# Kernel tuning notes

Measured on AMD Instinct MI355X. Metric: run time of the kernel, lower is better.

Reference implementation:

```python
import jax, jax.numpy as jnp
import numpy as np

L = 5          # number of pyramid levels (cat_fuse expects 5*C input channels)
C = 192        # in_channels, divisible by 3 and 2
C3 = C // 3
C2 = C // 2
B = 4
SIZES = [(192, 192), (96, 96), (48, 48), (24, 24), (12, 12)]  # x[1] is reference scale


def conv1x1(x, w, b):
    # 1x1 conv (+ folded eval-mode BN): x [n,cin,h,w], w [cout,cin], b [cout]
    return jnp.einsum('oc,nchw->nohw', w, x) + b[None, :, None, None]


def setup_inputs() -> dict:
    key = jax.random.key(0)
    ks = iter(jax.random.split(key, 40))
    inp = {}
    for i, (h, w) in enumerate(SIZES):
        inp[f'x{i}'] = jax.random.normal(next(ks), (B, C, h, w), jnp.float32)
    def wp(shape):
        return jax.random.normal(next(ks), shape, jnp.float32) * 0.05
    for nm, co, ci in [('k1', C3, C), ('k2', C3, C), ('k3', C3, C), ('q', C, C), ('v', C, C),
                       ('cf', C, L * C), ('e1', C2, C), ('e2', C, C2), ('r1', C2, C), ('r2', C, C2)]:
        inp['W_' + nm] = wp((co, ci))
        inp['b_' + nm] = wp((co,))
    inp['bn_s'] = 1.0 + wp((C,))   # standalone BN folded to affine scale
    inp['bn_t'] = wp((C,))         # standalone BN folded to affine shift
    return inp


def reference(x0, x1, x2, x3, x4,
              W_k1, b_k1, W_k2, b_k2, W_k3, b_k3,
              W_q, b_q, W_v, b_v, W_cf, b_cf,
              W_e1, b_e1, W_e2, b_e2, W_r1, b_r1, W_r2, b_r2,
              bn_s, bn_t):
    xs = [x0, x1, x2, x3, x4]
    b, _, h, w = x1.shape
    hw = h * w
    # bilinear resize to reference scale (torch F.interpolate align_corners=False)
    x_up = [x1 if i == 1 else jax.image.resize(x, (b, C, h, w), 'bilinear') for i, x in enumerate(xs)]
    Xf = jnp.stack(x_up).reshape(L * b, C, h, w)  # shared weights across levels -> batch them

    def emb(z):  # conv1x1 -> GELU(exact) -> conv1x1 (dropout is identity at eval)
        return conv1x1(jax.nn.gelu(conv1x1(z, W_e1, b_e1), approximate=False), W_e2, b_e2)

    la_res = None
    for k in range(5):
        # residual refinement: relu(bn(x + res_block(x)))
        r = conv1x1(jax.nn.relu(conv1x1(Xf, W_r1, b_r1)), W_r2, b_r2)
        Xf = jax.nn.relu((Xf + r) * bn_s[None, :, None, None] + bn_t[None, :, None, None])
        # query/value: per-level projection, split C into 3 chunks -> 15 'keys' per pixel
        Q = conv1x1(Xf, W_q, b_q).reshape(L, b, 3, C3, hw)
        Q = Q.transpose(1, 0, 2, 3, 4).reshape(b, 3 * L, C3, hw).transpose(0, 3, 2, 1)  # [b,hw,C3,15]
        V = conv1x1(Xf, W_v, b_v).reshape(L, b, 3, C3, hw)
        V = V.transpose(1, 0, 2, 3, 4).reshape(b, 3 * L, C3, hw).transpose(0, 3, 1, 2)  # [b,hw,15,C3]
        if k == 0:
            cat = Xf.reshape(L, b, C, h, w).transpose(1, 0, 2, 3, 4).reshape(b, L * C, h, w)
            la_res = emb(jax.nn.relu(conv1x1(cat, W_cf, b_cf)))
        refs = []
        for Wk, bk in ((W_k1, b_k1), (W_k2, b_k2), (W_k3, b_k3)):
            key_i = conv1x1(la_res, Wk, bk).reshape(b, C3, hw).transpose(0, 2, 1)       # [b,hw,C3]
            att = jax.nn.softmax(jnp.einsum('bpc,bpck->bpk', key_i, Q), axis=-1)        # [b,hw,15]
            ref = jnp.einsum('bpk,bpkc->bpc', att, V)                                   # [b,hw,C3]
            refs.append(ref.transpose(0, 2, 1).reshape(b, C3, h, w))
        la_res = emb(jnp.concatenate(refs, axis=1))
    return la_res
```

## Files before the change

kernel.cpp:

```cpp
#include <hip/hip_runtime.h>
#include <math.h>

typedef unsigned short u16;
typedef unsigned int   u32;
typedef __bf16 bf16x8 __attribute__((ext_vector_type(8)));
typedef float  f32x4  __attribute__((ext_vector_type(4)));

__device__ __forceinline__ float b2f(u16 u) {
    unsigned v = ((unsigned)u) << 16;
    return __uint_as_float(v);
}
__device__ __forceinline__ u16 f2b(float f) {
    unsigned x = __float_as_uint(f);
    unsigned r = (x + 0x7fffu + ((x >> 16) & 1u)) >> 16;
    return (u16)r;
}
__device__ __forceinline__ void fsplit(float v, u16& h, u16& l) {
    h = f2b(v);
    l = f2b(v - b2f(h));
}
__device__ __forceinline__ float h2f(u16 u) {
    union { u16 us; _Float16 h; } c; c.us = u; return (float)c.h;
}
__device__ __forceinline__ u16 f2h(float f) {
    union { u16 us; _Float16 h; } c; c.h = (_Float16)f; return c.us;
}
__device__ __forceinline__ float ldx(const void* p, size_t i, int f32m) {
    return f32m ? ((const float*)p)[i] : b2f(((const u16*)p)[i]);
}

__global__ void detect_dtype(const u16* __restrict__ x0, int* flag)
{
    int lane = threadIdx.x;
    int bad = 0;
    for (int i = lane; i < 1024; i += 64) {
        float v = b2f(x0[i]);
        if (!(fabsf(v) < 32768.f)) bad = 1;
    }
    unsigned long long m = __ballot(bad);
    if (lane == 0) flag[0] = (m != 0ULL) ? 1 : 0;
}

struct SrcPtrs {
    const void *wr1, *br1, *wr2, *br2, *wq, *bq, *wv, *bv, *wcf, *bcf;
    const void *we1, *be1, *we2, *be2, *wk1, *bk1, *wk2, *bk2, *wk3, *bk3;
    const void *bns, *bnt;
};
__global__ void pack_weights(SrcPtrs S, u16* __restrict__ Wh, u16* __restrict__ Wl,
                             float* __restrict__ Bias, const int* __restrict__ dflag)
{
    const int f32m = *dflag;
    int idx = blockIdx.x * 256 + threadIdx.x;
    if (idx < 368640) {
        const void* src; size_t si;
        if (idx < 18432)       { src = S.wr1; si = idx; }
        else if (idx < 36864)  { src = S.wr2; si = idx - 18432; }
        else if (idx < 110592) {
            int r = idx - 36864, o = r / 192, c = r % 192;
            if (o < 192) { src = S.wq; si = (size_t)o * 192 + c; }
            else         { src = S.wv; si = (size_t)(o - 192) * 192 + c; }
        }
        else if (idx < 294912) { src = S.wcf; si = idx - 110592; }
        else if (idx < 313344) { src = S.we1; si = idx - 294912; }
        else if (idx < 331776) { src = S.we2; si = idx - 313344; }
        else {
            int r = idx - 331776, o = r / 192, c = r % 192;
            src = (o < 64) ? S.wk1 : ((o < 128) ? S.wk2 : S.wk3);
            si = (size_t)(o & 63) * 192 + c;
        }
        u16 h, l; fsplit(ldx(src, si, f32m), h, l);
        Wh[idx] = h; Wl[idx] = l;
    } else if (idx < 370368) {
        int b = idx - 368640; const void* src; size_t si;
        if (b < 96)        { src = S.br1; si = b; }
        else if (b < 288)  { src = S.br2; si = b - 96; }
        else if (b < 672)  { int r = b - 288;
                             if (r < 192) { src = S.bq; si = r; }
                             else         { src = S.bv; si = r - 192; } }
        else if (b < 864)  { src = S.bcf; si = b - 672; }
        else if (b < 960)  { src = S.be1; si = b - 864; }
        else if (b < 1152) { src = S.be2; si = b - 960; }
        else if (b < 1344) { int r = b - 1152;
                             src = (r < 64) ? S.bk1 : ((r < 128) ? S.bk2 : S.bk3);
                             si = r & 63; }
        else if (b < 1536) { src = S.bns; si = b - 1344; }
        else               { src = S.bnt; si = b - 1536; }
        Bias[b] = ldx(src, si, f32m);
    }
}

__global__ void build_tables(float* __restrict__ wtab, int* __restrict__ jtab)
{
    int t = threadIdx.x;
    if (t >= 384) return;
    int li = t / 96, o = t % 96;
    const int ins[4] = {192, 48, 24, 12};
    int in = ins[li];
    float scale = (float)in / 96.0f;
    float ksc = fmaxf(scale, 1.0f);
    float cc = (o + 0.5f) * scale - 0.5f;
    float w[4] = {0.f, 0.f, 0.f, 0.f};
    int   j[4] = {0, 0, 0, 0};
    int n = 0; float s = 0.f;
    int jl = (int)floorf(cc - ksc), jh = (int)floorf(cc + ksc) + 1;
    for (int jj = jl; jj <= jh; jj++) {
        if (jj < 0 || jj >= in) continue;
        float ww = 1.0f - fabsf((float)jj - cc) / ksc;
        if (ww <= 0.f) continue;
        if (n < 4) { w[n] = ww; j[n] = jj; s += ww; n++; }
    }
    for (int i = 0; i < 4; i++) {
        wtab[li * 384 + o * 4 + i] = w[i] / s;
        jtab[li * 384 + o * 4 + i] = j[i];
    }
}

template<int SPLIT>
__launch_bounds__(256)
__global__ void transpose_in(const void* __restrict__ src, int HW,
                             u32* __restrict__ P, u16* __restrict__ Xh,
                             u16* __restrict__ Xl, const int* __restrict__ dflag)
{
    __shared__ float t[32][33];
    const int f32m = *dflag;
    const int b  = blockIdx.z;
    const int c0 = blockIdx.y * 32;
    const int p0 = blockIdx.x * 32;
    const int tid = threadIdx.x;
#pragma unroll
    for (int it = 0; it < 4; it++) {
        int i = it * 256 + tid;
        int pl = i & 31, cl = i >> 5;
        int p = p0 + pl;
        float v = 0.f;
        if (p < HW) v = ldx(src, ((size_t)(b * 192 + c0 + cl)) * HW + p, f32m);
        t[pl][cl] = v;
    }
    __syncthreads();
#pragma unroll
    for (int it = 0; it < 4; it++) {
        int i = it * 256 + tid;
        int cl = i & 31, pl = i >> 5;
        int p = p0 + pl;
        if (p >= HW) continue;
        float v = t[pl][cl];
        u16 h, l; fsplit(v, h, l);
        if constexpr (SPLIT) {
            size_t oi = ((size_t)((4 + b) * 9216 + p)) * 192 + c0 + cl;
            Xh[oi] = h; Xl[oi] = l;
        } else {
            P[((size_t)b * HW + p) * 192 + c0 + cl] = (u32)h | ((u32)l << 16);
        }
    }
}

template<int TAPS>
__launch_bounds__(256)
__global__ void upsample2(const u32* __restrict__ Pa, const u32* __restrict__ Pb,
                          const u32* __restrict__ Pc,
                          const float* __restrict__ wtab, const int* __restrict__ jtab,
                          u16* __restrict__ Xh, u16* __restrict__ Xl)
{
    int li, b, l, in;
    const u32* P;
    if constexpr (TAPS == 4) {
        li = 0; b = blockIdx.y; l = 0; in = 192; P = Pa;
    } else {
        int yi = blockIdx.y;
        li = 1 + (yi >> 2); b = yi & 3;
        const int lvl[4] = {0, 2, 3, 4};
        const int ins[4] = {192, 48, 24, 12};
        l = lvl[li]; in = ins[li];
        P = (li == 1) ? Pa : ((li == 2) ? Pb : Pc);
    }
    int gid = blockIdx.x * 256 + threadIdx.x;
    int c = gid % 192;
    int p = gid / 192;
    int y = p / 96, x = p % 96;
    const float* wt = wtab + li * 384;
    const int*   jt = jtab + li * 384;

    size_t ib = (size_t)b * in * in * 192 + c;
    float a = 0.f;
#pragma unroll
    for (int iy = 0; iy < TAPS; iy++) {
        float wy = wt[y * 4 + iy];
        size_t rb = ib + (size_t)(jt[y * 4 + iy] * in) * 192;
        float ax = 0.f;
#pragma unroll
        for (int ix = 0; ix < TAPS; ix++) {
            u32 u = P[rb + jt[x * 4 + ix] * 192];
            ax += wt[x * 4 + ix] * (b2f((u16)u) + b2f((u16)(u >> 16)));
        }
        a += wy * ax;
    }
    size_t oi = ((size_t)(l * 4 + b) * 9216 + p) * 192 + c;
    u16 h, lo; fsplit(a, h, lo);
    Xh[oi] = h; Xl[oi] = lo;
}

template<int MT, int NT, int ACT, int MODE, int OUT>
__launch_bounds__(256)
__global__ void conv_gemm(const u16* __restrict__ Ah, const u16* __restrict__ Al,
                          const u16* __restrict__ Wh, const u16* __restrict__ Wl,
                          const float* __restrict__ Bias,
                          int woff, int boff, int K, int O,
                          u16* __restrict__ out0, u16* __restrict__ out1)
{
    constexpr int BM = MT * 64, BN = NT * 16;
    __shared__ u16 Ash[BM * 40];
    __shared__ u16 Asl[BM * 40];
    __shared__ u16 Bsh[BN * 40];
    __shared__ u16 Bsl[BN * 40];

    const int tid  = threadIdx.x;
    const int lane = tid & 63, wave = tid >> 6;
    const int qd   = lane >> 4, ln = lane & 15;
    const int p0   = blockIdx.x * BM;
    const int img  = blockIdx.z;
    const int M    = 9216;

    f32x4 acc[MT][NT];
#pragma unroll
    for (int mt = 0; mt < MT; mt++)
#pragma unroll
        for (int j = 0; j < NT; j++) acc[mt][j] = (f32x4){0.f, 0.f, 0.f, 0.f};

    for (int kb = 0; kb < K; kb += 32) {
#pragma unroll
        for (int i = 0; i < MT; i++) {
            int idx = i * 256 + tid;
            int row = idx >> 2, ch = idx & 3;
            size_t base;
            if constexpr (MODE == 2) {
                int l = kb / 192, c0 = kb - l * 192 + ch * 8;
                base = ((size_t)((l * 4 + img) * M + p0 + row)) * 192 + c0;
            } else {
                base = ((size_t)(img * M + p0 + row)) * (size_t)K + kb + ch * 8;
            }
            *(float4*)&Ash[row * 40 + ch * 8] = *(const float4*)(Ah + base);
            *(float4*)&Asl[row * 40 + ch * 8] = *(const float4*)(Al + base);
        }
        constexpr int BI = (BN * 4) / 256;
#pragma unroll
        for (int i = 0; i < BI; i++) {
            int idx = i * 256 + tid;
            int row = idx >> 2, ch = idx & 3;
            size_t wb = (size_t)woff + (size_t)row * K + kb + ch * 8;
            *(float4*)&Bsh[row * 40 + ch * 8] = *(const float4*)(Wh + wb);
            *(float4*)&Bsl[row * 40 + ch * 8] = *(const float4*)(Wl + wb);
        }
        __syncthreads();
        bf16x8 ah[MT], al[MT];
#pragma unroll
        for (int mt = 0; mt < MT; mt++) {
            ah[mt] = *(const bf16x8*)&Ash[(wave * MT * 16 + mt * 16 + ln) * 40 + qd * 8];
            al[mt] = *(const bf16x8*)&Asl[(wave * MT * 16 + mt * 16 + ln) * 40 + qd * 8];
        }
#pragma unroll
        for (int j = 0; j < NT; j++) {
            bf16x8 bh = *(const bf16x8*)&Bsh[(j * 16 + ln) * 40 + qd * 8];
            bf16x8 bl = *(const bf16x8*)&Bsl[(j * 16 + ln) * 40 + qd * 8];
#pragma unroll
            for (int mt = 0; mt < MT; mt++) {
                acc[mt][j] = __builtin_amdgcn_mfma_f32_16x16x32_bf16(ah[mt], bh, acc[mt][j], 0, 0, 0);
                acc[mt][j] = __builtin_amdgcn_mfma_f32_16x16x32_bf16(ah[mt], bl, acc[mt][j], 0, 0, 0);
                acc[mt][j] = __builtin_amdgcn_mfma_f32_16x16x32_bf16(al[mt], bh, acc[mt][j], 0, 0, 0);
            }
        }
        __syncthreads();
    }

#pragma unroll
    for (int mt = 0; mt < MT; mt++) {
#pragma unroll
        for (int j = 0; j < NT; j++) {
            int o = j * 16 + ln;
            float bvf = Bias[boff + o];
#pragma unroll
            for (int r = 0; r < 4; r++) {
                int prow = p0 + wave * MT * 16 + mt * 16 + qd * 4 + r;
                float v = acc[mt][j][r] + bvf;
                if constexpr (ACT == 1) v = fmaxf(v, 0.f);
                if constexpr (OUT == 0) {
                    size_t oidx = ((size_t)(img * M + prow)) * (size_t)O + o;
                    u16 h, l; fsplit(v, h, l);
                    out0[oidx] = h; out1[oidx] = l;
                } else if constexpr (OUT == 1) {
                    out0[((size_t)(img * M + prow)) * (size_t)O + o] = f2h(v);
                } else {
                    size_t pb = ((size_t)(img * M + prow)) * 192;
                    if (o < 192) out0[pb + o] = f2h(v);
                    else         out1[pb + o - 192] = f2h(v);
                }
            }
        }
    }
}

template<int ACT1, int MODE2>
__launch_bounds__(256)
__global__ void fused_mlp(const u16* __restrict__ Ah, const u16* __restrict__ Al,
                          const u16* __restrict__ Wh, const u16* __restrict__ Wl,
                          const float* __restrict__ Bias,
                          int w1off, int b1off, int w2off, int b2off,
                          u16* __restrict__ outh, u16* __restrict__ outl)
{
    __shared__ u16 Hh[64 * 104];
    __shared__ u16 Hl[64 * 104];
    __shared__ u16 SB[15360];
    u16* B1h = SB;
    u16* B1l = SB + 3840;
    u16* As  = SB + 7680;
    u16* Asl = SB + 10240;

    const int tid  = threadIdx.x;
    const int lane = tid & 63, wave = tid >> 6;
    const int qd   = lane >> 4, ln = lane & 15;
    const int p0   = blockIdx.x * 64;
    const int img  = blockIdx.z;
    const int M    = 9216;

    f32x4 acc1[6];
#pragma unroll
    for (int j = 0; j < 6; j++) acc1[j] = (f32x4){0.f, 0.f, 0.f, 0.f};

    for (int kb = 0; kb < 192; kb += 32) {
        {
            int row = tid >> 2, ch = tid & 3;
            size_t base = ((size_t)(img * M + p0 + row)) * 192 + kb + ch * 8;
            *(float4*)&As[row * 40 + ch * 8]  = *(const float4*)(Ah + base);
            *(float4*)&Asl[row * 40 + ch * 8] = *(const float4*)(Al + base);
        }
#pragma unroll
        for (int i = 0; i < 2; i++) {
            int idx = i * 256 + tid;
            if (idx < 384) {
                int row = idx >> 2, ch = idx & 3;
                size_t wb = (size_t)w1off + (size_t)row * 192 + kb + ch * 8;
                *(float4*)&B1h[row * 40 + ch * 8] = *(const float4*)(Wh + wb);
                *(float4*)&B1l[row * 40 + ch * 8] = *(const float4*)(Wl + wb);
            }
        }
        __syncthreads();
        bf16x8 ah = *(const bf16x8*)&As[(wave * 16 + ln) * 40 + qd * 8];
        bf16x8 al = *(const bf16x8*)&Asl[(wave * 16 + ln) * 40 + qd * 8];
#pragma unroll
        for (int j = 0; j < 6; j++) {
            bf16x8 bh = *(const bf16x8*)&B1h[(j * 16 + ln) * 40 + qd * 8];
            bf16x8 bl = *(const bf16x8*)&B1l[(j * 16 + ln) * 40 + qd * 8];
            acc1[j] = __builtin_amdgcn_mfma_f32_16x16x32_bf16(ah, bh, acc1[j], 0, 0, 0);
            acc1[j] = __builtin_amdgcn_mfma_f32_16x16x32_bf16(ah, bl, acc1[j], 0, 0, 0);
            acc1[j] = __builtin_amdgcn_mfma_f32_16x16x32_bf16(al, bh, acc1[j], 0, 0, 0);
        }
        __syncthreads();
    }
#pragma unroll
    for (int j = 0; j < 6; j++) {
        int o = j * 16 + ln;
        float bvf = Bias[b1off + o];
#pragma unroll
        for (int r = 0; r < 4; r++) {
            float v = acc1[j][r] + bvf;
            if constexpr (ACT1 == 1) v = fmaxf(v, 0.f);
            if constexpr (ACT1 == 2) v = 0.5f * v * (1.f + erff(v * 0.70710678118654752f));
            u16 h, l; fsplit(v, h, l);
            int row = wave * 16 + qd * 4 + r;
            Hh[row * 104 + o] = h;
            Hl[row * 104 + o] = l;
        }
    }
    __syncthreads();

    u16* B2h = SB;
    u16* B2l = SB + 7680;
    f32x4 acc2[12];
#pragma unroll
    for (int j = 0; j < 12; j++) acc2[j] = (f32x4){0.f, 0.f, 0.f, 0.f};

    for (int kb = 0; kb < 96; kb += 32) {
#pragma unroll
        for (int i = 0; i < 3; i++) {
            int idx = i * 256 + tid;
            int row = idx >> 2, ch = idx & 3;
            size_t wb = (size_t)w2off + (size_t)row * 96 + kb + ch * 8;
            *(float4*)&B2h[row * 40 + ch * 8] = *(const float4*)(Wh + wb);
            *(float4*)&B2l[row * 40 + ch * 8] = *(const float4*)(Wl + wb);
        }
        __syncthreads();
        bf16x8 ah = *(const bf16x8*)&Hh[(wave * 16 + ln) * 104 + kb + qd * 8];
        bf16x8 al = *(const bf16x8*)&Hl[(wave * 16 + ln) * 104 + kb + qd * 8];
#pragma unroll
        for (int j = 0; j < 12; j++) {
            bf16x8 bh = *(const bf16x8*)&B2h[(j * 16 + ln) * 40 + qd * 8];
            bf16x8 bl = *(const bf16x8*)&B2l[(j * 16 + ln) * 40 + qd * 8];
            acc2[j] = __builtin_amdgcn_mfma_f32_16x16x32_bf16(ah, bh, acc2[j], 0, 0, 0);
            acc2[j] = __builtin_amdgcn_mfma_f32_16x16x32_bf16(ah, bl, acc2[j], 0, 0, 0);
            acc2[j] = __builtin_amdgcn_mfma_f32_16x16x32_bf16(al, bh, acc2[j], 0, 0, 0);
        }
        __syncthreads();
    }

#pragma unroll
    for (int j = 0; j < 12; j++) {
        int o = j * 16 + ln;
        float bvf = Bias[b2off + o];
#pragma unroll
        for (int r = 0; r < 4; r++) {
            int prow = p0 + wave * 16 + qd * 4 + r;
            float v = acc2[j][r] + bvf;
            size_t oidx = ((size_t)(img * M + prow)) * 192 + o;
            if constexpr (MODE2 == 1) {
                float xo = b2f(outh[oidx]) + b2f(outl[oidx]);
                v = fmaxf((xo + v) * Bias[1344 + o] + Bias[1536 + o], 0.f);
            }
            u16 h, l; fsplit(v, h, l);
            outh[oidx] = h; outl[oidx] = l;
        }
    }
}

template<int WRITE_X>
__launch_bounds__(256)
__global__ void fused_res_qv(u16* __restrict__ Xh, u16* __restrict__ Xl,
                             const u16* __restrict__ Wh, const u16* __restrict__ Wl,
                             const float* __restrict__ Bias,
                             u16* __restrict__ Qf, u16* __restrict__ Vf)
{
    __shared__ __align__(16) u16 LDS[39936];
    u16* Hh  = LDS;
    u16* Hl  = LDS + 6656;
    u16* SB  = LDS + 13312;
    u16* B1h = SB;
    u16* B1l = SB + 3840;
    u16* As  = SB + 7680;
    u16* Asl = SB + 10240;

    const int tid  = threadIdx.x;
    const int lane = tid & 63, wave = tid >> 6;
    const int qd   = lane >> 4, ln = lane & 15;
    const int p0   = blockIdx.x * 64;
    const int img  = blockIdx.z;
    const int M    = 9216;

    f32x4 acc1[6];
#pragma unroll
    for (int j = 0; j < 6; j++) acc1[j] = (f32x4){0.f, 0.f, 0.f, 0.f};

    for (int kb = 0; kb < 192; kb += 32) {
        {
            int row = tid >> 2, ch = tid & 3;
            size_t base = ((size_t)(img * M + p0 + row)) * 192 + kb + ch * 8;
            *(float4*)&As[row * 40 + ch * 8]  = *(const float4*)(Xh + base);
            *(float4*)&Asl[row * 40 + ch * 8] = *(const float4*)(Xl + base);
        }
#pragma unroll
        for (int i = 0; i < 2; i++) {
            int idx = i * 256 + tid;
            if (idx < 384) {
                int row = idx >> 2, ch = idx & 3;
                size_t wb = (size_t)row * 192 + kb + ch * 8;
                *(float4*)&B1h[row * 40 + ch * 8] = *(const float4*)(Wh + wb);
                *(float4*)&B1l[row * 40 + ch * 8] = *(const float4*)(Wl + wb);
            }
        }
        __syncthreads();
        bf16x8 ah = *(const bf16x8*)&As[(wave * 16 + ln) * 40 + qd * 8];
        bf16x8 al = *(const bf16x8*)&Asl[(wave * 16 + ln) * 40 + qd * 8];
#pragma unroll
        for (int j = 0; j < 6; j++) {
            bf16x8 bh = *(const bf16x8*)&B1h[(j * 16 + ln) * 40 + qd * 8];
            bf16x8 bl = *(const bf16x8*)&B1l[(j * 16 + ln) * 40 + qd * 8];
            acc1[j] = __builtin_amdgcn_mfma_f32_16x16x32_bf16(ah, bh, acc1[j], 0, 0, 0);
            acc1[j] = __builtin_amdgcn_mfma_f32_16x16x32_bf16(ah, bl, acc1[j], 0, 0, 0);
            acc1[j] = __builtin_amdgcn_mfma_f32_16x16x32_bf16(al, bh, acc1[j], 0, 0, 0);
        }
        __syncthreads();
    }
#pragma unroll
    for (int j = 0; j < 6; j++) {
        int o = j * 16 + ln;
        float bvf = Bias[o];
#pragma unroll
        for (int r = 0; r < 4; r++) {
            float v = fmaxf(acc1[j][r] + bvf, 0.f);
            u16 h, l; fsplit(v, h, l);
            int row = wave * 16 + qd * 4 + r;
            Hh[row * 104 + o] = h;
            Hl[row * 104 + o] = l;
        }
    }
    __syncthreads();

    u16* B2h = SB;
    u16* B2l = SB + 7680;
    f32x4 acc2[12];
#pragma unroll
    for (int j = 0; j < 12; j++) acc2[j] = (f32x4){0.f, 0.f, 0.f, 0.f};

    for (int kb = 0; kb < 96; kb += 32) {
#pragma unroll
        for (int i = 0; i < 3; i++) {
            int idx = i * 256 + tid;
            int row = idx >> 2, ch = idx & 3;
            size_t wb = (size_t)18432 + (size_t)row * 96 + kb + ch * 8;
            *(float4*)&B2h[row * 40 + ch * 8] = *(const float4*)(Wh + wb);
            *(float4*)&B2l[row * 40 + ch * 8] = *(const float4*)(Wl + wb);
        }
        __syncthreads();
        bf16x8 ah = *(const bf16x8*)&Hh[(wave * 16 + ln) * 104 + kb + qd * 8];
        bf16x8 al = *(const bf16x8*)&Hl[(wave * 16 + ln) * 104 + kb + qd * 8];
#pragma unroll
        for (int j = 0; j < 12; j++) {
            bf16x8 bh = *(const bf16x8*)&B2h[(j * 16 + ln) * 40 + qd * 8];
            bf16x8 bl = *(const bf16x8*)&B2l[(j * 16 + ln) * 40 + qd * 8];
            acc2[j] = __builtin_amdgcn_mfma_f32_16x16x32_bf16(ah, bh, acc2[j], 0, 0, 0);
            acc2[j] = __builtin_amdgcn_mfma_f32_16x16x32_bf16(ah, bl, acc2[j], 0, 0, 0);
            acc2[j] = __builtin_amdgcn_mfma_f32_16x16x32_bf16(al, bh, acc2[j], 0, 0, 0);
        }
        __syncthreads();
    }

    u16* X2h = LDS;
    u16* X2l = LDS + 12288;
#pragma unroll
    for (int j = 0; j < 12; j++) {
        int o = j * 16 + ln;
        float bvf = Bias[96 + o];
#pragma unroll
        for (int r = 0; r < 4; r++) {
            int row  = wave * 16 + qd * 4 + r;
            int prow = p0 + row;
            float v = acc2[j][r] + bvf;
            size_t oidx = ((size_t)(img * M + prow)) * 192 + o;
            float xo = b2f(Xh[oidx]) + b2f(Xl[oidx]);
            v = fmaxf((xo + v) * Bias[1344 + o] + Bias[1536 + o], 0.f);
            u16 h, l; fsplit(v, h, l);
            if constexpr (WRITE_X) { Xh[oidx] = h; Xl[oidx] = l; }
            int off = ((row * 192 + o) * 2) ^ ((row & 7) << 4);
            *(u16*)((char*)X2h + off) = h;
            *(u16*)((char*)X2l + off) = l;
        }
    }
    __syncthreads();

    u16* B3h = LDS + 24576;
    u16* B3l = LDS + 32256;
    const int arow = wave * 16 + ln;
#pragma unroll 1
    for (int pass = 0; pass < 2; pass++) {
        f32x4 acc3[12];
#pragma unroll
        for (int j = 0; j < 12; j++) acc3[j] = (f32x4){0.f, 0.f, 0.f, 0.f};

        for (int kb = 0; kb < 192; kb += 32) {
#pragma unroll
            for (int i = 0; i < 3; i++) {
                int idx = i * 256 + tid;
                int row = idx >> 2, ch = idx & 3;
                size_t wb = (size_t)36864 + (size_t)(pass * 192 + row) * 192 + kb + ch * 8;
                *(float4*)&B3h[row * 40 + ch * 8] = *(const float4*)(Wh + wb);
                *(float4*)&B3l[row * 40 + ch * 8] = *(const float4*)(Wl + wb);
            }
            __syncthreads();
            int aoff = ((arow * 192 + kb + qd * 8) * 2) ^ ((arow & 7) << 4);
            bf16x8 ah = *(const bf16x8*)((const char*)X2h + aoff);
            bf16x8 al = *(const bf16x8*)((const char*)X2l + aoff);
#pragma unroll
            for (int j = 0; j < 12; j++) {
                bf16x8 bh = *(const bf16x8*)&B3h[(j * 16 + ln) * 40 + qd * 8];
                bf16x8 bl = *(const bf16x8*)&B3l[(j * 16 + ln) * 40 + qd * 8];
                acc3[j] = __builtin_amdgcn_mfma_f32_16x16x32_bf16(ah, bh, acc3[j], 0, 0, 0);
                acc3[j] = __builtin_amdgcn_mfma_f32_16x16x32_bf16(ah, bl, acc3[j], 0, 0, 0);
                acc3[j] = __builtin_amdgcn_mfma_f32_16x16x32_bf16(al, bh, acc3[j], 0, 0, 0);
            }
            __syncthreads();
        }
#pragma unroll
        for (int j = 0; j < 12; j++) {
            int o = pass * 192 + j * 16 + ln;
            float bvf = Bias[288 + o];
#pragma unroll
            for (int r = 0; r < 4; r++) {
                int prow = p0 + wave * 16 + qd * 4 + r;
                float v = acc3[j][r] + bvf;
                u16 q = f2h(v);
                size_t pb = ((size_t)(img * M + prow)) * 192;
                if (o < 192) Qf[pb + o] = q;
                else         Vf[pb + o - 192] = q;
            }
        }
    }
}

__global__ void attn_kernel(const u16* __restrict__ Qb, const u16* __restrict__ Vb,
                            const u16* __restrict__ Keys,
                            u16* __restrict__ Rh, u16* __restrict__ Rl)
{
    const int lane = threadIdx.x & 63;
    const int wv   = threadIdx.x >> 6;
    const int p = blockIdx.x * 4 + wv;
    const int b = blockIdx.y;

    float qv[15], vv[15];
#pragma unroll
    for (int l = 0; l < 5; l++) {
        size_t base = ((size_t)((l * 4 + b) * 9216 + p)) * 192;
#pragma unroll
        for (int j = 0; j < 3; j++) {
            qv[l * 3 + j] = h2f(Qb[base + j * 64 + lane]);
            vv[l * 3 + j] = h2f(Vb[base + j * 64 + lane]);
        }
    }
    size_t kb = ((size_t)(b * 9216 + p)) * 192;
#pragma unroll
    for (int i = 0; i < 3; i++) {
        float kf = h2f(Keys[kb + i * 64 + lane]);
        float lg[15];
#pragma unroll
        for (int t = 0; t < 15; t++) {
            float s = kf * qv[t];
#pragma unroll
            for (int m = 1; m < 64; m <<= 1) s += __shfl_xor(s, m, 64);
            lg[t] = s;
        }
        float mx = lg[0];
#pragma unroll
        for (int t = 1; t < 15; t++) mx = fmaxf(mx, lg[t]);
        float sum = 0.f;
#pragma unroll
        for (int t = 0; t < 15; t++) { lg[t] = __expf(lg[t] - mx); sum += lg[t]; }
        float inv = 1.f / sum;
        float ref = 0.f;
#pragma unroll
        for (int t = 0; t < 15; t++) ref += lg[t] * vv[t];
        u16 h, lo; fsplit(ref * inv, h, lo);
        Rh[kb + i * 64 + lane] = h;
        Rl[kb + i * 64 + lane] = lo;
    }
}

__launch_bounds__(256)
__global__ void transpose_out(const u16* __restrict__ Lah, const u16* __restrict__ Lal,
                              float* __restrict__ out)
{
    __shared__ float t[32][33];
    const int b  = blockIdx.z;
    const int c0 = blockIdx.y * 32;
    const int p0 = blockIdx.x * 32;
    const int tid = threadIdx.x;
#pragma unroll
    for (int it = 0; it < 4; it++) {
        int i = it * 256 + tid;
        int cl = i & 31, pl = i >> 5;
        size_t idx = ((size_t)(b * 9216 + p0 + pl)) * 192 + c0 + cl;
        t[pl][cl] = b2f(Lah[idx]) + b2f(Lal[idx]);
    }
    __syncthreads();
#pragma unroll
    for (int it = 0; it < 4; it++) {
        int i = it * 256 + tid;
        int pl = i & 31, cl = i >> 5;
        out[((size_t)(b * 192 + c0 + cl)) * 9216 + p0 + pl] = t[pl][cl];
    }
}

__global__ void ws_too_small_kernel(float* out)
{
    int gid = blockIdx.x * 256 + threadIdx.x;
    out[gid] = 12345.0f;
}

extern "C" void kernel_launch(void* const* d_in, const int* in_sizes, int n_in,
                              void* d_out, int out_size, void* d_ws, size_t ws_size,
                              hipStream_t stream)
{
    u16* ws = (u16*)d_ws;
    const size_t oXh   = 0;
    const size_t oXl   = 35389440;
    const size_t oQ    = 70778880;
    const size_t oV    = 106168320;
    const size_t oLah  = 141557760;
    const size_t oLal  = 148635648;
    const size_t oKeys = 155713536;
    const size_t oRh   = 162791424;
    const size_t oRl   = 169869312;
    const size_t oWh   = 176947200;
    const size_t oWl   = 177315840;
    const size_t oBias = 177684480;
    const size_t oWtab = 177687936;
    const size_t oJtab = 177691008;
    const size_t oFlag = 177694080;
    const size_t need_bytes = (size_t)177694096 * 2;

    if (ws_size < need_bytes) {
        ws_too_small_kernel<<<dim3(out_size / 256), dim3(256), 0, stream>>>((float*)d_out);
        return;
    }

    u16* Xh   = ws + oXh;
    u16* Xl   = ws + oXl;
    u16* Qf   = ws + oQ;
    u16* Vf   = ws + oV;
    u16* Lah  = ws + oLah;
    u16* Lal  = ws + oLal;
    u16* Keys = ws + oKeys;
    u16* Rh   = ws + oRh;
    u16* Rl   = ws + oRl;
    u16* Wh   = ws + oWh;
    u16* Wl   = ws + oWl;
    float* Bias = (float*)(ws + oBias);
    float* wtab = (float*)(ws + oWtab);
    int*   jtab = (int*)(ws + oJtab);
    int*   flag = (int*)(ws + oFlag);

    u32* P0 = (u32*)(ws + oQ);
    u32* P2 = (u32*)(ws + oLah);
    u32* P3 = (u32*)(ws + oLal);
    u32* P4 = (u32*)(ws + oKeys);

    SrcPtrs S;
    S.wk1 = d_in[5];  S.bk1 = d_in[6];
    S.wk2 = d_in[7];  S.bk2 = d_in[8];
    S.wk3 = d_in[9];  S.bk3 = d_in[10];
    S.wq  = d_in[11]; S.bq  = d_in[12];
    S.wv  = d_in[13]; S.bv  = d_in[14];
    S.wcf = d_in[15]; S.bcf = d_in[16];
    S.we1 = d_in[17]; S.be1 = d_in[18];
    S.we2 = d_in[19]; S.be2 = d_in[20];
    S.wr1 = d_in[21]; S.br1 = d_in[22];
    S.wr2 = d_in[23]; S.br2 = d_in[24];
    S.bns = d_in[25]; S.bnt = d_in[26];

    dim3 blk(256);
    detect_dtype<<<dim3(1), dim3(64), 0, stream>>>((const u16*)d_in[0], flag);
    pack_weights<<<dim3(1447), blk, 0, stream>>>(S, Wh, Wl, Bias, flag);
    build_tables<<<dim3(1), dim3(384), 0, stream>>>(wtab, jtab);

    transpose_in<0><<<dim3(1152, 6, 4), blk, 0, stream>>>(d_in[0], 36864, P0, nullptr, nullptr, flag);
    transpose_in<1><<<dim3( 288, 6, 4), blk, 0, stream>>>(d_in[1],  9216, nullptr, Xh, Xl, flag);
    transpose_in<0><<<dim3(  72, 6, 4), blk, 0, stream>>>(d_in[2],  2304, P2, nullptr, nullptr, flag);
    transpose_in<0><<<dim3(  18, 6, 4), blk, 0, stream>>>(d_in[3],   576, P3, nullptr, nullptr, flag);
    transpose_in<0><<<dim3(   5, 6, 4), blk, 0, stream>>>(d_in[4],   144, P4, nullptr, nullptr, flag);
    upsample2<4><<<dim3(6912,  4), blk, 0, stream>>>(P0, nullptr, nullptr, wtab, jtab, Xh, Xl);
    upsample2<2><<<dim3(6912, 12), blk, 0, stream>>>(P2, P3, P4, wtab, jtab, Xh, Xl);

    for (int k = 0; k < 5; k++) {
        if (k < 4)
            fused_res_qv<1><<<dim3(144, 1, 20), blk, 0, stream>>>(
                Xh, Xl, Wh, Wl, Bias, Qf, Vf);
        else
            fused_res_qv<0><<<dim3(144, 1, 20), blk, 0, stream>>>(
                Xh, Xl, Wh, Wl, Bias, Qf, Vf);
        if (k == 0) {
            conv_gemm<2, 12, 1, 2, 0><<<dim3(72, 1, 4), blk, 0, stream>>>(
                Xh, Xl, Wh, Wl, Bias, 110592, 672, 960, 192, Rh, Rl);
            fused_mlp<2, 0><<<dim3(144, 1, 4), blk, 0, stream>>>(
                Rh, Rl, Wh, Wl, Bias, 294912, 864, 313344, 960, Lah, Lal);
        }
        conv_gemm<2, 12, 0, 0, 1><<<dim3(72, 1, 4), blk, 0, stream>>>(
            Lah, Lal, Wh, Wl, Bias, 331776, 1152, 192, 192, Keys, nullptr);
        attn_kernel<<<dim3(2304, 4), blk, 0, stream>>>(Qf, Vf, Keys, Rh, Rl);
        fused_mlp<2, 0><<<dim3(144, 1, 4), blk, 0, stream>>>(
            Rh, Rl, Wh, Wl, Bias, 294912, 864, 313344, 960, Lah, Lal);
    }
    transpose_out<<<dim3(288, 6, 4), blk, 0, stream>>>(Lah, Lal, (float*)d_out);
}
```

Measured before the change: 2.801 ms.

## Load GEMM operands directly from global memory into MFMA registers, bypassing LDS staging

The conv GEMM and fused MLP kernels now load A activations and B weights straight from global memory into bf16x8 fragments instead of staging them through shared memory. This removes the per-k-step __syncthreads barriers and the LDS write/read round trip, and lowers LDS use, which can raise occupancy. In exchange, weight tiles are re-read by every wave through L1/L2 instead of being shared once per block. The per-lane 16-byte row-strided loads may coalesce worse, and global latency is exposed with no explicit prefetch.

Result: slower. 4.997 ms (+78.4%).

```diff
diff --git a/kernel.cpp b/kernel.cpp
--- a/kernel.cpp
+++ b/kernel.cpp
@@ -207,12 +207,7 @@
                           int woff, int boff, int K, int O,
                           u16* __restrict__ out0, u16* __restrict__ out1)
 {
-    constexpr int BM = MT * 64, BN = NT * 16;
-    __shared__ u16 Ash[BM * 40];
-    __shared__ u16 Asl[BM * 40];
-    __shared__ u16 Bsh[BN * 40];
-    __shared__ u16 Bsl[BN * 40];
-
+    constexpr int BM = MT * 64;
     const int tid  = threadIdx.x;
     const int lane = tid & 63, wave = tid >> 6;
     const int qd   = lane >> 4, ln = lane & 15;
@@ -227,40 +222,25 @@
         for (int j = 0; j < NT; j++) acc[mt][j] = (f32x4){0.f, 0.f, 0.f, 0.f};
 
     for (int kb = 0; kb < K; kb += 32) {
-#pragma unroll
-        for (int i = 0; i < MT; i++) {
-            int idx = i * 256 + tid;
-            int row = idx >> 2, ch = idx & 3;
+        bf16x8 ah[MT], al[MT];
+#pragma unroll
+        for (int mt = 0; mt < MT; mt++) {
+            int row = wave * MT * 16 + mt * 16 + ln;
             size_t base;
             if constexpr (MODE == 2) {
-                int l = kb / 192, c0 = kb - l * 192 + ch * 8;
-                base = ((size_t)((l * 4 + img) * M + p0 + row)) * 192 + c0;
+                int l = kb / 192;
+                base = ((size_t)((l * 4 + img) * M + p0 + row)) * 192 + (kb - l * 192) + qd * 8;
             } else {
-                base = ((size_t)(img * M + p0 + row)) * (size_t)K + kb + ch * 8;
+                base = ((size_t)(img * M + p0 + row)) * (size_t)K + kb + qd * 8;
             }
-            *(float4*)&Ash[row * 40 + ch * 8] = *(const float4*)(Ah + base);
-            *(float4*)&Asl[row * 40 + ch * 8] = *(const float4*)(Al + base);
-        }
-        constexpr int BI = (BN * 4) / 256;
-#pragma unroll
-        for (int i = 0; i < BI; i++) {
-            int idx = i * 256 + tid;
-            int row = idx >> 2, ch = idx & 3;
-            size_t wb = (size_t)woff + (size_t)row * K + kb + ch * 8;
-            *(float4*)&Bsh[row * 40 + ch * 8] = *(const float4*)(Wh + wb);
-            *(float4*)&Bsl[row * 40 + ch * 8] = *(const float4*)(Wl + wb);
-        }
-        __syncthreads();
-        bf16x8 ah[MT], al[MT];
-#pragma unroll
-        for (int mt = 0; mt < MT; mt++) {
-            ah[mt] = *(const bf16x8*)&Ash[(wave * MT * 16 + mt * 16 + ln) * 40 + qd * 8];
-            al[mt] = *(const bf16x8*)&Asl[(wave * MT * 16 + mt * 16 + ln) * 40 + qd * 8];
+            ah[mt] = *(const bf16x8*)(Ah + base);
+            al[mt] = *(const bf16x8*)(Al + base);
         }
 #pragma unroll
         for (int j = 0; j < NT; j++) {
-            bf16x8 bh = *(const bf16x8*)&Bsh[(j * 16 + ln) * 40 + qd * 8];
-            bf16x8 bl = *(const bf16x8*)&Bsl[(j * 16 + ln) * 40 + qd * 8];
+            size_t wb = (size_t)woff + (size_t)(j * 16 + ln) * K + kb + qd * 8;
+            bf16x8 bh = *(const bf16x8*)(Wh + wb);
+            bf16x8 bl = *(const bf16x8*)(Wl + wb);
 #pragma unroll
             for (int mt = 0; mt < MT; mt++) {
                 acc[mt][j] = __builtin_amdgcn_mfma_f32_16x16x32_bf16(ah[mt], bh, acc[mt][j], 0, 0, 0);
@@ -268,7 +248,6 @@
                 acc[mt][j] = __builtin_amdgcn_mfma_f32_16x16x32_bf16(al[mt], bh, acc[mt][j], 0, 0, 0);
             }
         }
-        __syncthreads();
     }
 
 #pragma unroll
@@ -308,11 +287,6 @@
 {
     __shared__ u16 Hh[64 * 104];
     __shared__ u16 Hl[64 * 104];
-    __shared__ u16 SB[15360];
-    u16* B1h = SB;
-    u16* B1l = SB + 3840;
-    u16* As  = SB + 7680;
-    u16* Asl = SB + 10240;
 
     const int tid  = threadIdx.x;
     const int lane = tid & 63, wave = tid >> 6;
@@ -321,39 +295,25 @@
     const int img  = blockIdx.z;
     const int M    = 9216;
 
+    const size_t abase = ((size_t)(img * M + p0 + wave * 16 + ln)) * 192 + qd * 8;
+
     f32x4 acc1[6];
 #pragma unroll
     for (int j = 0; j < 6; j++) acc1[j] = (f32x4){0.f, 0.f, 0.f, 0.f};
 
+#pragma unroll 2
     for (int kb = 0; kb < 192; kb += 32) {
-        {
-            int row = tid >> 2, ch = tid & 3;
-            size_t base = ((size_t)(img * M + p0 + row)) * 192 + kb + ch * 8;
-            *(float4*)&As[row * 40 + ch * 8]  = *(const float4*)(Ah + base);
-            *(float4*)&Asl[row * 40 + ch * 8] = *(const float4*)(Al + base);
-        }
-#pragma unroll
-        for (int i = 0; i < 2; i++) {
-            int idx = i * 256 + tid;
-            if (idx < 384) {
-                int row = idx >> 2, ch = idx & 3;
-                size_t wb = (size_t)w1off + (size_t)row * 192 + kb + ch * 8;
-                *(float4*)&B1h[row * 40 + ch * 8] = *(const float4*)(Wh + wb);
-                *(float4*)&B1l[row * 40 + ch * 8] = *(const float4*)(Wl + wb);
-            }
-        }
-        __syncthreads();
-        bf16x8 ah = *(const bf16x8*)&As[(wave * 16 + ln) * 40 + qd * 8];
-        bf16x8 al = *(const bf16x8*)&Asl[(wave * 16 + ln) * 40 + qd * 8];
+        bf16x8 ah = *(const bf16x8*)(Ah + abase + kb);
+        bf16x8 al = *(const bf16x8*)(Al + abase + kb);
 #pragma unroll
         for (int j = 0; j < 6; j++) {
-            bf16x8 bh = *(const bf16x8*)&B1h[(j * 16 + ln) * 40 + qd * 8];
-            bf16x8 bl = *(const bf16x8*)&B1l[(j * 16 + ln) * 40 + qd * 8];
+            size_t wb = (size_t)w1off + (size_t)(j * 16 + ln) * 192 + kb + qd * 8;
+            bf16x8 bh = *(const bf16x8*)(Wh + wb);
+            bf16x8 bl = *(const bf16x8*)(Wl + wb);
             acc1[j] = __builtin_amdgcn_mfma_f32_16x16x32_bf16(ah, bh, acc1[j], 0, 0, 0);
             acc1[j] = __builtin_amdgcn_mfma_f32_16x16x32_bf16(ah, bl, acc1[j], 0, 0, 0);
             acc1[j] = __builtin_amdgcn_mfma_f32_16x16x32_bf16(al, bh, acc1[j], 0, 0, 0);
         }
-        __syncthreads();
     }
 #pragma unroll
     for (int j = 0; j < 6; j++) {
@@ -372,33 +332,23 @@
     }
     __syncthreads();
 
-    u16* B2h = SB;
-    u16* B2l = SB + 7680;
     f32x4 acc2[12];
 #pragma unroll
     for (int j = 0; j < 12; j++) acc2[j] = (f32x4){0.f, 0.f, 0.f, 0.f};
 
+#pragma unroll
     for (int kb = 0; kb < 96; kb += 32) {
-#pragma unroll
-        for (int i = 0; i < 3; i++) {
-            int idx = i * 256 + tid;
-            int row = idx >> 2, ch = idx & 3;
-            size_t wb = (size_t)w2off + (size_t)row * 96 + kb + ch * 8;
-            *(float4*)&B2h[row * 40 + ch * 8] = *(const float4*)(Wh + wb);
-            *(float4*)&B2l[row * 40 + ch * 8] = *(const float4*)(Wl + wb);
-        }
-        __syncthreads();
         bf16x8 ah = *(const bf16x8*)&Hh[(wave * 16 + ln) * 104 + kb + qd * 8];
         bf16x8 al = *(const bf16x8*)&Hl[(wave * 16 + ln) * 104 + kb + qd * 8];
 #pragma unroll
         for (int j = 0; j < 12; j++) {
-            bf16x8 bh = *(const bf16x8*)&B2h[(j * 16 + ln) * 40 + qd * 8];
-            bf16x8 bl = *(const bf16x8*)&B2l[(j * 16 + ln) * 40 + qd * 8];
+            size_t wb = (size_t)w2off + (size_t)(j * 16 + ln) * 96 + kb + qd * 8;
+            bf16x8 bh = *(const bf16x8*)(Wh + wb);
+            bf16x8 bl = *(const bf16x8*)(Wl + wb);
             acc2[j] = __builtin_amdgcn_mfma_f32_16x16x32_bf16(ah, bh, acc2[j], 0, 0, 0);
             acc2[j] = __builtin_amdgcn_mfma_f32_16x16x32_bf16(ah, bl, acc2[j], 0, 0, 0);
             acc2[j] = __builtin_amdgcn_mfma_f32_16x16x32_bf16(al, bh, acc2[j], 0, 0, 0);
         }
-        __syncthreads();
     }
 
 #pragma unroll
@@ -427,14 +377,9 @@
                              const float* __restrict__ Bias,
                              u16* __restrict__ Qf, u16* __restrict__ Vf)
 {
-    __shared__ __align__(16) u16 LDS[39936];
+    __shared__ __align__(16) u16 LDS[24576];
     u16* Hh  = LDS;
     u16* Hl  = LDS + 6656;
-    u16* SB  = LDS + 13312;
-    u16* B1h = SB;
-    u16* B1l = SB + 3840;
-    u16* As  = SB + 7680;
-    u16* Asl = SB + 10240;
 
     const int tid  = threadIdx.x;
     const int lane = tid & 63, wave = tid >> 6;
@@ -443,39 +388,25 @@
     const int img  = blockIdx.z;
     const int M    = 9216;
 
+    const size_t abase = ((size_t)(img * M + p0 + wave * 16 + ln)) * 192 + qd * 8;
+
     f32x4 acc1[6];
 #pragma unroll
     for (int j = 0; j < 6; j++) acc1[j] = (f32x4){0.f, 0.f, 0.f, 0.f};
 
+#pragma unroll 2
     for (int kb = 0; kb < 192; kb += 32) {
-        {
-            int row = tid >> 2, ch = tid & 3;
-            size_t base = ((size_t)(img * M + p0 + row)) * 192 + kb + ch * 8;
-            *(float4*)&As[row * 40 + ch * 8]  = *(const float4*)(Xh + base);
-            *(float4*)&Asl[row * 40 + ch * 8] = *(const float4*)(Xl + base);
-        }
-#pragma unroll
-        for (int i = 0; i < 2; i++) {
-            int idx = i * 256 + tid;
-            if (idx < 384) {
-                int row = idx >> 2, ch = idx & 3;
-                size_t wb = (size_t)row * 192 + kb + ch * 8;
-                *(float4*)&B1h[row * 40 + ch * 8] = *(const float4*)(Wh + wb);
-                *(float4*)&B1l[row * 40 + ch * 8] = *(const float4*)(Wl + wb);
-            }
-        }
-        __syncthreads();
-        bf16x8 ah = *(const bf16x8*)&As[(wave * 16 + ln) * 40 + qd * 8];
-        bf16x8 al = *(const bf16x8*)&Asl[(wave * 16 + ln) * 40 + qd * 8];
+        bf16x8 ah = *(const bf16x8*)(Xh + abase + kb);
+        bf16x8 al = *(const bf16x8*)(Xl + abase + kb);
 #pragma unroll
         for (int j = 0; j < 6; j++) {
-            bf16x8 bh = *(const bf16x8*)&B1h[(j * 16 + ln) * 40 + qd * 8];
-            bf16x8 bl = *(const bf16x8*)&B1l[(j * 16 + ln) * 40 + qd * 8];
+            size_t wb = (size_t)(j * 16 + ln) * 192 + kb + qd * 8;
+            bf16x8 bh = *(const bf16x8*)(Wh + wb);
+            bf16x8 bl = *(const bf16x8*)(Wl + wb);
             acc1[j] = __builtin_amdgcn_mfma_f32_16x16x32_bf16(ah, bh, acc1[j], 0, 0, 0);
             acc1[j] = __builtin_amdgcn_mfma_f32_16x16x32_bf16(ah, bl, acc1[j], 0, 0, 0);
             acc1[j] = __builtin_amdgcn_mfma_f32_16x16x32_bf16(al, bh, acc1[j], 0, 0, 0);
         }
-        __syncthreads();
     }
 #pragma unroll
     for (int j = 0; j < 6; j++) {
@@ -492,34 +423,25 @@
     }
     __syncthreads();
 
-    u16* B2h = SB;
-    u16* B2l = SB + 7680;
     f32x4 acc2[12];
 #pragma unroll
     for (int j = 0; j < 12; j++) acc2[j] = (f32x4){0.f, 0.f, 0.f, 0.f};
 
+#pragma unroll
     for (int kb = 0; kb < 96; kb += 32) {
-#pragma unroll
-        for (int i = 0; i < 3; i++) {
-            int idx = i * 256 + tid;
-            int row = idx >> 2, ch = idx & 3;
-            size_t wb = (size_t)18432 + (size_t)row * 96 + kb + ch * 8;
-            *(float4*)&B2h[row * 40 + ch * 8] = *(const float4*)(Wh + wb);
-            *(float4*)&B2l[row * 40 + ch * 8] = *(const float4*)(Wl + wb);
-        }
-        __syncthreads();
         bf16x8 ah = *(const bf16x8*)&Hh[(wave * 16 + ln) * 104 + kb + qd * 8];
         bf16x8 al = *(const bf16x8*)&Hl[(wave * 16 + ln) * 104 + kb + qd * 8];
 #pragma unroll
         for (int j = 0; j < 12; j++) {
-            bf16x8 bh = *(const bf16x8*)&B2h[(j * 16 + ln) * 40 + qd * 8];
-            bf16x8 bl = *(const bf16x8*)&B2l[(j * 16 + ln) * 40 + qd * 8];
+            size_t wb = (size_t)18432 + (size_t)(j * 16 + ln) * 96 + kb + qd * 8;
+            bf16x8 bh = *(const bf16x8*)(Wh + wb);
+            bf16x8 bl = *(const bf16x8*)(Wl + wb);
             acc2[j] = __builtin_amdgcn_mfma_f32_16x16x32_bf16(ah, bh, acc2[j], 0, 0, 0);
             acc2[j] = __builtin_amdgcn_mfma_f32_16x16x32_bf16(ah, bl, acc2[j], 0, 0, 0);
             acc2[j] = __builtin_amdgcn_mfma_f32_16x16x32_bf16(al, bh, acc2[j], 0, 0, 0);
         }
-        __syncthreads();
-    }
+    }
+    __syncthreads();
 
     u16* X2h = LDS;
     u16* X2l = LDS + 12288;
@@ -544,8 +466,6 @@
     }
     __syncthreads();
 
-    u16* B3h = LDS + 24576;
-    u16* B3l = LDS + 32256;
     const int arow = wave * 16 + ln;
 #pragma unroll 1
     for (int pass = 0; pass < 2; pass++) {
@@ -553,28 +473,20 @@
 #pragma unroll
         for (int j = 0; j < 12; j++) acc3[j] = (f32x4){0.f, 0.f, 0.f, 0.f};
 
+#pragma unroll 2
         for (int kb = 0; kb < 192; kb += 32) {
-#pragma unroll
-            for (int i = 0; i < 3; i++) {
-                int idx = i * 256 + tid;
-                int row = idx >> 2, ch = idx & 3;
-                size_t wb = (size_t)36864 + (size_t)(pass * 192 + row) * 192 + kb + ch * 8;
-                *(float4*)&B3h[row * 40 + ch * 8] = *(const float4*)(Wh + wb);
-                *(float4*)&B3l[row * 40 + ch * 8] = *(const float4*)(Wl + wb);
-            }
-            __syncthreads();
             int aoff = ((arow * 192 + kb + qd * 8) * 2) ^ ((arow & 7) << 4);
             bf16x8 ah = *(const bf16x8*)((const char*)X2h + aoff);
             bf16x8 al = *(const bf16x8*)((const char*)X2l + aoff);
 #pragma unroll
             for (int j = 0; j < 12; j++) {
-                bf16x8 bh = *(const bf16x8*)&B3h[(j * 16 + ln) * 40 + qd * 8];
-                bf16x8 bl = *(const bf16x8*)&B3l[(j * 16 + ln) * 40 + qd * 8];
+                size_t wb = (size_t)36864 + (size_t)(pass * 192 + j * 16 + ln) * 192 + kb + qd * 8;
+                bf16x8 bh = *(const bf16x8*)(Wh + wb);
+                bf16x8 bl = *(const bf16x8*)(Wl + wb);
                 acc3[j] = __builtin_amdgcn_mfma_f32_16x16x32_bf16(ah, bh, acc3[j], 0, 0, 0);
                 acc3[j] = __builtin_amdgcn_mfma_f32_16x16x32_bf16(ah, bl, acc3[j], 0, 0, 0);
                 acc3[j] = __builtin_amdgcn_mfma_f32_16x16x32_bf16(al, bh, acc3[j], 0, 0, 0);
             }
-            __syncthreads();
         }
 #pragma unroll
         for (int j = 0; j < 12; j++) {
```
